# Performance work log

Measured on AMD Instinct MI355X. Metric: run time of the kernel, lower is better.

## Reference

```python
import jax, jax.numpy as jnp
import numpy as np
from jax import lax

WINDOW_SIZE = 11
SIGMA = 1.5
DATA_RANGE = 1.0
C1 = (0.01 * DATA_RANGE) ** 2
C2 = (0.03 * DATA_RANGE) ** 2


def _gaussian_window(channels: int) -> jnp.ndarray:
    coords = jnp.arange(WINDOW_SIZE, dtype=jnp.float32) - (WINDOW_SIZE // 2)
    g = jnp.exp(-coords ** 2 / (2.0 * SIGMA ** 2))
    g = g / g.sum()
    k2d = jnp.outer(g, g)  # [K, K]
    # depthwise kernel [C, 1, K, K] (OIHW with feature_group_count=C)
    return jnp.broadcast_to(k2d[None, None], (channels, 1, WINDOW_SIZE, WINDOW_SIZE))


def _depthwise_conv(x: jnp.ndarray, window: jnp.ndarray) -> jnp.ndarray:
    pad = WINDOW_SIZE // 2
    return lax.conv_general_dilated(
        x, window,
        window_strides=(1, 1),
        padding=[(pad, pad), (pad, pad)],
        dimension_numbers=("NCHW", "OIHW", "NCHW"),
        feature_group_count=x.shape[1],
    )


def setup_inputs() -> dict:
    key = jax.random.key(0)
    k1, k2 = jax.random.split(key)
    shape = (16, 3, 512, 512)
    pred = jax.random.uniform(k1, shape, dtype=jnp.float32)
    target = jax.random.uniform(k2, shape, dtype=jnp.float32)
    return {"pred": pred, "target": target}


def reference(pred, target):
    channels = pred.shape[1]
    window = _gaussian_window(channels)

    mu1 = _depthwise_conv(pred, window)
    mu2 = _depthwise_conv(target, window)
    mu1_sq = mu1 ** 2
    mu2_sq = mu2 ** 2
    mu1_mu2 = mu1 * mu2

    sigma1_sq = _depthwise_conv(pred * pred, window) - mu1_sq
    sigma2_sq = _depthwise_conv(target * target, window) - mu2_sq
    sigma12 = _depthwise_conv(pred * target, window) - mu1_mu2

    ssim_map = ((2.0 * mu1_mu2 + C1) * (2.0 * sigma12 + C2)) / (
        (mu1_sq + mu2_sq + C1) * (sigma1_sq + sigma2_sq + C2)
    )
    return 1.0 - ssim_map.mean()
```

## Files before the change

### kernel.cpp

```cpp
#include <hip/hip_runtime.h>
#include <cmath>

#define HH 512
#define WW 512
#define TW 32
#define TH 64
#define INH 74
#define TWP 33
#define NTHREADS 512
#define NXT 16
#define NYT 8
#define NPL 48
#define NBLK (NXT * NYT * NPL)
#define C1F 0.0001f
#define C2F 0.0009f

typedef float v2f __attribute__((ext_vector_type(2)));

struct GaussW { float w[11]; };

__device__ __forceinline__ void load16a4(const float* __restrict__ p, float v[16]) {
    *(float4*)&v[0]  = *(const float4*)(p);
    *(float4*)&v[4]  = *(const float4*)(p + 4);
    *(float4*)&v[8]  = *(const float4*)(p + 8);
    *(float4*)&v[12] = *(const float4*)(p + 12);
}
__device__ __forceinline__ void load16a2(const float* __restrict__ p, float v[16]) {
    *(float2*)&v[0]  = *(const float2*)(p);
    *(float4*)&v[2]  = *(const float4*)(p + 2);
    *(float4*)&v[6]  = *(const float4*)(p + 6);
    *(float4*)&v[10] = *(const float4*)(p + 10);
    *(float2*)&v[14] = *(const float2*)(p + 14);
}

__global__ __launch_bounds__(NTHREADS) void ssim_tile_kernel(
    const float* __restrict__ pred, const float* __restrict__ targ,
    float* __restrict__ partial, GaussW gw)
{
    __shared__ __align__(16) float hp[INH][TWP][4];
    __shared__ float wred[8];

    const int tid = threadIdx.x;

    const int lid = (blockIdx.z * gridDim.y + blockIdx.y) * gridDim.x + blockIdx.x;
    const int wi  = (lid & 7) * (NBLK / 8) + (lid >> 3);
    const int bx  = wi & (NXT - 1);
    const int by  = (wi >> 4) & (NYT - 1);
    const int bz  = wi >> 7;

    const int gx0 = bx * TW;
    const int gy0 = by * TH - 5;
    const size_t plane = (size_t)bz * (size_t)(HH * WW);

    const bool lblk = (bx == 0);
    const bool rblk = (bx == NXT - 1);

    for (int i = tid; i < INH * 8; i += NTHREADS) {
        int r = i >> 3;
        int g = i & 7;
        int c0 = g << 2;
        int gr = gy0 + r;

        if ((unsigned)gr >= (unsigned)HH) {
            float4 z = make_float4(0.f, 0.f, 0.f, 0.f);
            #pragma unroll
            for (int o = 0; o < 4; o++) {
                int phys = (g ^ (o << 1)) + (o << 3);
                *(float4*)&hp[r][phys][0] = z;
            }
            continue;
        }

        const float* prow = pred + plane + (size_t)gr * WW;
        const float* trow = targ + plane + (size_t)gr * WW;

        v2f ab[14];
        if (lblk && g < 2) {
            float P[16], T[16];
            load16a4(prow, P);
            load16a4(trow, T);
            if (g == 0) {
                #pragma unroll
                for (int j = 0; j < 14; j++) {
                    float pv = (j >= 5) ? P[j - 5] : 0.f;
                    float tv = (j >= 5) ? T[j - 5] : 0.f;
                    ab[j] = (v2f){pv + tv, pv - tv};
                }
            } else {
                #pragma unroll
                for (int j = 0; j < 14; j++) {
                    float pv = (j >= 1) ? P[j - 1] : 0.f;
                    float tv = (j >= 1) ? T[j - 1] : 0.f;
                    ab[j] = (v2f){pv + tv, pv - tv};
                }
            }
        } else if (rblk && g > 5) {
            float P[16], T[16];
            load16a4(prow + (WW - 16), P);
            load16a4(trow + (WW - 16), T);
            if (g == 6) {
                #pragma unroll
                for (int j = 0; j < 14; j++) {
                    float pv = (j <= 12) ? P[j + 3] : 0.f;
                    float tv = (j <= 12) ? T[j + 3] : 0.f;
                    ab[j] = (v2f){pv + tv, pv - tv};
                }
            } else {
                #pragma unroll
                for (int j = 0; j < 14; j++) {
                    float pv = (j <= 8) ? P[j + 7] : 0.f;
                    float tv = (j <= 8) ? T[j + 7] : 0.f;
                    ab[j] = (v2f){pv + tv, pv - tv};
                }
            }
        } else {
            float P[16], T[16];
            load16a2(prow + gx0 + c0 - 6, P);
            load16a2(trow + gx0 + c0 - 6, T);
            #pragma unroll
            for (int j = 0; j < 14; j++) {
                float pv = P[j + 1], tv = T[j + 1];
                ab[j] = (v2f){pv + tv, pv - tv};
            }
        }

        v2f s1[4], s2[4];
        #pragma unroll
        for (int o = 0; o < 4; o++) { s1[o] = (v2f)(0.f); s2[o] = (v2f)(0.f); }
        #pragma unroll
        for (int j = 0; j < 14; j++) {
            v2f v  = ab[j];
            v2f v2 = v * v;
            #pragma unroll
            for (int o = 0; o < 4; o++) {
                int k = j - o;
                if (k >= 0 && k < 11) {
                    float wk = gw.w[k];
                    s1[o] += wk * v;
                    s2[o] += wk * v2;
                }
            }
        }
        #pragma unroll
        for (int o = 0; o < 4; o++) {
            int phys = (g ^ (o << 1)) + (o << 3);
            *(float4*)&hp[r][phys][0] =
                make_float4(s1[o].x, s1[o].y, s2[o].x, s2[o].y);
        }
    }
    __syncthreads();

    float local = 0.f;
    {
        const int c0 = tid & 31;
        const int r0 = (tid >> 5) << 2;
        const int pc = ((c0 >> 2) ^ ((c0 & 3) << 1)) + ((c0 & 3) << 3);
        const float* hbase = &hp[r0][pc][0];

        v2f accm[4], acce[4];
        #pragma unroll
        for (int rr = 0; rr < 4; rr++) { accm[rr] = (v2f)(0.f); acce[rr] = (v2f)(0.f); }

        #pragma unroll
        for (int jj = 0; jj < 14; jj++) {
            float4 v = *(const float4*)(hbase + (size_t)jj * (TWP * 4));
            v2f vm = (v2f){v.x, v.y};
            v2f ve = (v2f){v.z, v.w};
            #pragma unroll
            for (int rr = 0; rr < 4; rr++) {
                int k = jj - rr;
                if (k >= 0 && k < 11) {
                    float wk = gw.w[k];
                    accm[rr] += wk * vm;
                    acce[rr] += wk * ve;
                }
            }
        }

        #pragma unroll
        for (int rr = 0; rr < 4; rr++) {
            float A  = accm[rr].x, Bv = accm[rr].y;
            float EA = acce[rr].x, EB = acce[rr].y;
            float A2 = A * A, B2 = Bv * Bv;
            float S  = 0.5f  * (A2 + B2);
            float P  = 0.25f * (A2 - B2);
            float Ep = 0.5f  * (EA + EB);
            float Ec = 0.25f * (EA - EB);
            float num = (2.f * P + C1F) * (2.f * (Ec - P) + C2F);
            float den = (S + C1F) * ((Ep - S) + C2F);
            local += num * __builtin_amdgcn_rcpf(den);
        }
    }

    #pragma unroll
    for (int off = 32; off > 0; off >>= 1)
        local += __shfl_down(local, off, 64);
    int lane = tid & 63, wid = tid >> 6;
    if (lane == 0) wred[wid] = local;
    __syncthreads();
    if (tid == 0) {
        float s = 0.f;
        #pragma unroll
        for (int w2 = 0; w2 < 8; w2++) s += wred[w2];
        partial[lid] = s;
    }
}

__global__ __launch_bounds__(256) void ssim_finalize_kernel(
    const float* __restrict__ partial, float inv_count,
    float* __restrict__ out)
{
    __shared__ float sm[4];
    float s = 0.f;
    #pragma unroll
    for (int i = 0; i < NBLK / 4 / 256; i++) {
        float4 v = *(const float4*)&partial[(threadIdx.x + i * 256) * 4];
        s += (v.x + v.y) + (v.z + v.w);
    }
    #pragma unroll
    for (int off = 32; off > 0; off >>= 1)
        s += __shfl_down(s, off, 64);
    int lane = threadIdx.x & 63, wid = threadIdx.x >> 6;
    if (lane == 0) sm[wid] = s;
    __syncthreads();
    if (threadIdx.x == 0)
        out[0] = 1.0f - (sm[0] + sm[1] + sm[2] + sm[3]) * inv_count;
}

extern "C" void kernel_launch(void* const* d_in, const int* in_sizes, int n_in,
                              void* d_out, int out_size, void* d_ws, size_t ws_size,
                              hipStream_t stream)
{
    const float* pred = (const float*)d_in[0];
    const float* targ = (const float*)d_in[1];
    float* out = (float*)d_out;
    float* partial = (float*)d_ws;

    const int total = in_sizes[0];

    GaussW gw;
    double g[11], s = 0.0;
    for (int i = 0; i < 11; i++) {
        double d = (double)(i - 5);
        g[i] = exp(-d * d / 4.5);
        s += g[i];
    }
    for (int i = 0; i < 11; i++) gw.w[i] = (float)(g[i] / s);

    dim3 grid(NXT, NYT, NPL);
    ssim_tile_kernel<<<grid, NTHREADS, 0, stream>>>(pred, targ, partial, gw);

    const float inv_count = 1.0f / (float)total;
    ssim_finalize_kernel<<<1, 256, 0, stream>>>(partial, inv_count, out);
}
```

Measured before the change: 140.0 us.

## Process two vertical tiles per block, reusing the 10-row halo in shared memory

Each block now covers two stacked 64-row tiles, so half as many blocks are launched. After the first tile's vertical pass, the 10 halo rows at the bottom of shared memory are copied to the top, and only 64 new rows are horizontally convolved from global memory. This removes the redundant halo loads and horizontal convolutions for the shared rows. In exchange it adds two extra barriers, serialises the two tiles inside each block, and halves the grid size, which may reduce latency hiding.

```diff
diff --git a/kernel.cpp b/kernel.cpp
--- a/kernel.cpp
+++ b/kernel.cpp
@@ -9,7 +9,7 @@
 #define TWP 33
 #define NTHREADS 512
 #define NXT 16
-#define NYT 8
+#define NYT 4
 #define NPL 48
 #define NBLK (NXT * NYT * NPL)
 #define C1F 0.0001f
@@ -33,6 +33,147 @@
     *(float2*)&v[14] = *(const float2*)(p + 14);
 }
 
+
+__device__ __forceinline__ void conv_task(
+    const float* __restrict__ pred, const float* __restrict__ targ,
+    size_t plane, int gx0, bool lblk, bool rblk,
+    int r, int g, int gr, const GaussW& gw,
+    float (&hp)[INH][TWP][4])
+{
+    if ((unsigned)gr >= (unsigned)HH) {
+        float4 z = make_float4(0.f, 0.f, 0.f, 0.f);
+        #pragma unroll
+        for (int o = 0; o < 4; o++) {
+            int phys = (g ^ (o << 1)) + (o << 3);
+            *(float4*)&hp[r][phys][0] = z;
+        }
+        return;
+    }
+
+    const float* prow = pred + plane + (size_t)gr * WW;
+    const float* trow = targ + plane + (size_t)gr * WW;
+    const int c0 = g << 2;
+
+    v2f ab[14];
+    if (lblk && g < 2) {
+        float P[16], T[16];
+        load16a4(prow, P);
+        load16a4(trow, T);
+        if (g == 0) {
+            #pragma unroll
+            for (int j = 0; j < 14; j++) {
+                float pv = (j >= 5) ? P[j - 5] : 0.f;
+                float tv = (j >= 5) ? T[j - 5] : 0.f;
+                ab[j] = (v2f){pv + tv, pv - tv};
+            }
+        } else {
+            #pragma unroll
+            for (int j = 0; j < 14; j++) {
+                float pv = (j >= 1) ? P[j - 1] : 0.f;
+                float tv = (j >= 1) ? T[j - 1] : 0.f;
+                ab[j] = (v2f){pv + tv, pv - tv};
+            }
+        }
+    } else if (rblk && g > 5) {
+        float P[16], T[16];
+        load16a4(prow + (WW - 16), P);
+        load16a4(trow + (WW - 16), T);
+        if (g == 6) {
+            #pragma unroll
+            for (int j = 0; j < 14; j++) {
+                float pv = (j <= 12) ? P[j + 3] : 0.f;
+                float tv = (j <= 12) ? T[j + 3] : 0.f;
+                ab[j] = (v2f){pv + tv, pv - tv};
+            }
+        } else {
+            #pragma unroll
+            for (int j = 0; j < 14; j++) {
+                float pv = (j <= 8) ? P[j + 7] : 0.f;
+                float tv = (j <= 8) ? T[j + 7] : 0.f;
+                ab[j] = (v2f){pv + tv, pv - tv};
+            }
+        }
+    } else {
+        float P[16], T[16];
+        load16a2(prow + gx0 + c0 - 6, P);
+        load16a2(trow + gx0 + c0 - 6, T);
+        #pragma unroll
+        for (int j = 0; j < 14; j++) {
+            float pv = P[j + 1], tv = T[j + 1];
+            ab[j] = (v2f){pv + tv, pv - tv};
+        }
+    }
+
+    v2f s1[4], s2[4];
+    #pragma unroll
+    for (int o = 0; o < 4; o++) { s1[o] = (v2f)(0.f); s2[o] = (v2f)(0.f); }
+    #pragma unroll
+    for (int j = 0; j < 14; j++) {
+        v2f v  = ab[j];
+        v2f v2 = v * v;
+        #pragma unroll
+        for (int o = 0; o < 4; o++) {
+            int k = j - o;
+            if (k >= 0 && k < 11) {
+                float wk = gw.w[k];
+                s1[o] += wk * v;
+                s2[o] += wk * v2;
+            }
+        }
+    }
+    #pragma unroll
+    for (int o = 0; o < 4; o++) {
+        int phys = (g ^ (o << 1)) + (o << 3);
+        *(float4*)&hp[r][phys][0] =
+            make_float4(s1[o].x, s1[o].y, s2[o].x, s2[o].y);
+    }
+}
+
+__device__ __forceinline__ float phase_c(
+    const float (&hp)[INH][TWP][4], int tid, const GaussW& gw)
+{
+    const int c0 = tid & 31;
+    const int r0 = (tid >> 5) << 2;
+    const int pc = ((c0 >> 2) ^ ((c0 & 3) << 1)) + ((c0 & 3) << 3);
+    const float* hbase = &hp[r0][pc][0];
+
+    v2f accm[4], acce[4];
+    #pragma unroll
+    for (int rr = 0; rr < 4; rr++) { accm[rr] = (v2f)(0.f); acce[rr] = (v2f)(0.f); }
+
+    #pragma unroll
+    for (int jj = 0; jj < 14; jj++) {
+        float4 v = *(const float4*)(hbase + (size_t)jj * (TWP * 4));
+        v2f vm = (v2f){v.x, v.y};
+        v2f ve = (v2f){v.z, v.w};
+        #pragma unroll
+        for (int rr = 0; rr < 4; rr++) {
+            int k = jj - rr;
+            if (k >= 0 && k < 11) {
+                float wk = gw.w[k];
+                accm[rr] += wk * vm;
+                acce[rr] += wk * ve;
+            }
+        }
+    }
+
+    float local = 0.f;
+    #pragma unroll
+    for (int rr = 0; rr < 4; rr++) {
+        float A  = accm[rr].x, Bv = accm[rr].y;
+        float EA = acce[rr].x, EB = acce[rr].y;
+        float A2 = A * A, B2 = Bv * Bv;
+        float S  = 0.5f  * (A2 + B2);
+        float P  = 0.25f * (A2 - B2);
+        float Ep = 0.5f  * (EA + EB);
+        float Ec = 0.25f * (EA - EB);
+        float num = (2.f * P + C1F) * (2.f * (Ec - P) + C2F);
+        float den = (S + C1F) * ((Ep - S) + C2F);
+        local += num * __builtin_amdgcn_rcpf(den);
+    }
+    return local;
+}
+
 __global__ __launch_bounds__(NTHREADS) void ssim_tile_kernel(
     const float* __restrict__ pred, const float* __restrict__ targ,
     float* __restrict__ partial, GaussW gw)
@@ -46,151 +187,43 @@
     const int wi  = (lid & 7) * (NBLK / 8) + (lid >> 3);
     const int bx  = wi & (NXT - 1);
     const int by  = (wi >> 4) & (NYT - 1);
-    const int bz  = wi >> 7;
+    const int bz  = wi >> 6;
 
     const int gx0 = bx * TW;
-    const int gy0 = by * TH - 5;
+    const int gy0 = by * (2 * TH) - 5;
     const size_t plane = (size_t)bz * (size_t)(HH * WW);
 
     const bool lblk = (bx == 0);
     const bool rblk = (bx == NXT - 1);
 
-    for (int i = tid; i < INH * 8; i += NTHREADS) {
-        int r = i >> 3;
-        int g = i & 7;
-        int c0 = g << 2;
-        int gr = gy0 + r;
-
-        if ((unsigned)gr >= (unsigned)HH) {
-            float4 z = make_float4(0.f, 0.f, 0.f, 0.f);
-            #pragma unroll
-            for (int o = 0; o < 4; o++) {
-                int phys = (g ^ (o << 1)) + (o << 3);
-                *(float4*)&hp[r][phys][0] = z;
-            }
-            continue;
-        }
-
-        const float* prow = pred + plane + (size_t)gr * WW;
-        const float* trow = targ + plane + (size_t)gr * WW;
-
-        v2f ab[14];
-        if (lblk && g < 2) {
-            float P[16], T[16];
-            load16a4(prow, P);
-            load16a4(trow, T);
-            if (g == 0) {
-                #pragma unroll
-                for (int j = 0; j < 14; j++) {
-                    float pv = (j >= 5) ? P[j - 5] : 0.f;
-                    float tv = (j >= 5) ? T[j - 5] : 0.f;
-                    ab[j] = (v2f){pv + tv, pv - tv};
-                }
-            } else {
-                #pragma unroll
-                for (int j = 0; j < 14; j++) {
-                    float pv = (j >= 1) ? P[j - 1] : 0.f;
-                    float tv = (j >= 1) ? T[j - 1] : 0.f;
-                    ab[j] = (v2f){pv + tv, pv - tv};
-                }
-            }
-        } else if (rblk && g > 5) {
-            float P[16], T[16];
-            load16a4(prow + (WW - 16), P);
-            load16a4(trow + (WW - 16), T);
-            if (g == 6) {
-                #pragma unroll
-                for (int j = 0; j < 14; j++) {
-                    float pv = (j <= 12) ? P[j + 3] : 0.f;
-                    float tv = (j <= 12) ? T[j + 3] : 0.f;
-                    ab[j] = (v2f){pv + tv, pv - tv};
-                }
-            } else {
-                #pragma unroll
-                for (int j = 0; j < 14; j++) {
-                    float pv = (j <= 8) ? P[j + 7] : 0.f;
-                    float tv = (j <= 8) ? T[j + 7] : 0.f;
-                    ab[j] = (v2f){pv + tv, pv - tv};
-                }
-            }
-        } else {
-            float P[16], T[16];
-            load16a2(prow + gx0 + c0 - 6, P);
-            load16a2(trow + gx0 + c0 - 6, T);
-            #pragma unroll
-            for (int j = 0; j < 14; j++) {
-                float pv = P[j + 1], tv = T[j + 1];
-                ab[j] = (v2f){pv + tv, pv - tv};
-            }
-        }
-
-        v2f s1[4], s2[4];
-        #pragma unroll
-        for (int o = 0; o < 4; o++) { s1[o] = (v2f)(0.f); s2[o] = (v2f)(0.f); }
-        #pragma unroll
-        for (int j = 0; j < 14; j++) {
-            v2f v  = ab[j];
-            v2f v2 = v * v;
-            #pragma unroll
-            for (int o = 0; o < 4; o++) {
-                int k = j - o;
-                if (k >= 0 && k < 11) {
-                    float wk = gw.w[k];
-                    s1[o] += wk * v;
-                    s2[o] += wk * v2;
-                }
-            }
-        }
+    float local = 0.f;
+
+    for (int i = tid; i < INH * 8; i += NTHREADS)
+        conv_task(pred, targ, plane, gx0, lblk, rblk,
+                  i >> 3, i & 7, gy0 + (i >> 3), gw, hp);
+    __syncthreads();
+
+    local += phase_c(hp, tid, gw);
+    __syncthreads();
+
+    if (tid < 80) {
+        int r = tid >> 3, g = tid & 7;
         #pragma unroll
         for (int o = 0; o < 4; o++) {
             int phys = (g ^ (o << 1)) + (o << 3);
-            *(float4*)&hp[r][phys][0] =
-                make_float4(s1[o].x, s1[o].y, s2[o].x, s2[o].y);
-        }
-    }
-    __syncthreads();
-
-    float local = 0.f;
+            *(float4*)&hp[r][phys][0] = *(const float4*)&hp[64 + r][phys][0];
+        }
+    }
+    __syncthreads();
+
     {
-        const int c0 = tid & 31;
-        const int r0 = (tid >> 5) << 2;
-        const int pc = ((c0 >> 2) ^ ((c0 & 3) << 1)) + ((c0 & 3) << 3);
-        const float* hbase = &hp[r0][pc][0];
-
-        v2f accm[4], acce[4];
-        #pragma unroll
-        for (int rr = 0; rr < 4; rr++) { accm[rr] = (v2f)(0.f); acce[rr] = (v2f)(0.f); }
-
-        #pragma unroll
-        for (int jj = 0; jj < 14; jj++) {
-            float4 v = *(const float4*)(hbase + (size_t)jj * (TWP * 4));
-            v2f vm = (v2f){v.x, v.y};
-            v2f ve = (v2f){v.z, v.w};
-            #pragma unroll
-            for (int rr = 0; rr < 4; rr++) {
-                int k = jj - rr;
-                if (k >= 0 && k < 11) {
-                    float wk = gw.w[k];
-                    accm[rr] += wk * vm;
-                    acce[rr] += wk * ve;
-                }
-            }
-        }
-
-        #pragma unroll
-        for (int rr = 0; rr < 4; rr++) {
-            float A  = accm[rr].x, Bv = accm[rr].y;
-            float EA = acce[rr].x, EB = acce[rr].y;
-            float A2 = A * A, B2 = Bv * Bv;
-            float S  = 0.5f  * (A2 + B2);
-            float P  = 0.25f * (A2 - B2);
-            float Ep = 0.5f  * (EA + EB);
-            float Ec = 0.25f * (EA - EB);
-            float num = (2.f * P + C1F) * (2.f * (Ec - P) + C2F);
-            float den = (S + C1F) * ((Ep - S) + C2F);
-            local += num * __builtin_amdgcn_rcpf(den);
-        }
-    }
+        int r = 10 + (tid >> 3), g = tid & 7;
+        conv_task(pred, targ, plane, gx0, lblk, rblk,
+                  r, g, gy0 + 64 + r, gw, hp);
+    }
+    __syncthreads();
+
+    local += phase_c(hp, tid, gw);
 
     #pragma unroll
     for (int off = 32; off > 0; off >>= 1)
```

Measured after the change: 148.2 us. 1.06x slower.
